# Optimization experiments

Measured on AMD Instinct MI355X. Metric: run time of the kernel, lower is better.

## Reference

```python
import jax, jax.numpy as jnp
import numpy as np

LEAK_RATE = 0.1
SPIKE_THRESHOLD = 0.5
MAX_DIM = 2560
R = 2048   # reservoir dim
D = 1024   # input dim
B = 4096   # batch


def setup_inputs() -> dict:
    key = jax.random.key(0)
    k1, k2, k3, k4, k5 = jax.random.split(key, 5)
    inputs = jax.random.normal(k1, (B, D), dtype=jnp.float32)
    prev_state = jax.random.normal(k2, (B, MAX_DIM), dtype=jnp.float32)
    W_in = jax.random.normal(k3, (R, D), dtype=jnp.float32) * (1.0 / np.sqrt(D))
    W_res = jax.random.normal(k4, (R, R), dtype=jnp.float32) * (1.0 / np.sqrt(R))
    W_gate = jax.random.normal(k5, (3 * R, D), dtype=jnp.float32) * (1.0 / np.sqrt(D))
    return {"inputs": inputs, "prev_state": prev_state,
            "W_in": W_in, "W_res": W_res, "W_gate": W_gate}


def reference(inputs, prev_state, W_in, W_res, W_gate):
    # Slice state to active reservoir width (W_res.shape[0] == R)
    prev = prev_state[:, :R]                                  # [B, R]
    input_part = jnp.matmul(inputs, W_in.T)                   # [B, R]
    reservoir_part = jnp.matmul(prev, W_res.T)                # [B, R]
    gate = jax.nn.sigmoid(jnp.matmul(inputs, W_gate.T))       # [B, 3R]
    i_gate, f_gate, o_gate = jnp.split(gate, 3, axis=-1)      # each [B, R]
    state = (1.0 - LEAK_RATE) * (f_gate * prev) \
        + LEAK_RATE * jnp.tanh(i_gate * (input_part + reservoir_part))
    state = o_gate * state
    # Spike threshold + soft reset
    state = jnp.where(state > SPIKE_THRESHOLD, state - SPIKE_THRESHOLD, state)
    # Pad up to max dynamic reservoir dim
    padded = jnp.pad(state, ((0, 0), (0, MAX_DIM - R)))       # [B, MAX_DIM]
    return padded
```

## Files before the change

kernel.cpp:

```cpp
#include <hip/hip_runtime.h>

#define B_  4096
#define D_  1024
#define R_  2048
#define MAXD 2560

typedef _Float16 half8 __attribute__((ext_vector_type(8)));
typedef _Float16 half4 __attribute__((ext_vector_type(4)));
typedef float    f32x4 __attribute__((ext_vector_type(4)));

constexpr int BM = 128;
constexpr int BN = 64;
constexpr int BK = 32;
constexpr int NCHUNK = (D_ + R_) / BK;
constexpr int NCH1   = D_ / BK;

__device__ __forceinline__ float sigmoidf_(float x) { return 1.0f / (1.0f + expf(-x)); }

__device__ __forceinline__ void wg_barrier() {
    __builtin_amdgcn_sched_barrier(0);
    asm volatile("s_waitcnt lgkmcnt(0)" ::: "memory");
    __builtin_amdgcn_s_barrier();
    __builtin_amdgcn_sched_barrier(0);
}

__global__ __launch_bounds__(256, 2)
void reservoir_fused(const float* __restrict__ X,
                     const float* __restrict__ P,
                     const float* __restrict__ Win,
                     const float* __restrict__ Wres,
                     const float* __restrict__ Wg,
                     float* __restrict__ out)
{
    __shared__ _Float16 sA[2][8][512];
    __shared__ _Float16 sW[2][4][4][512];

    const int tid  = threadIdx.x;
    const int lane = tid & 63;
    const int wv   = tid >> 6;
    const int m0   = blockIdx.y * BM;
    const int n0   = blockIdx.x * BN;

    f32x4 acc[4][2][4];
    #pragma unroll
    for (int s = 0; s < 4; ++s)
        #pragma unroll
        for (int mt = 0; mt < 2; ++mt)
            #pragma unroll
            for (int nt = 0; nt < 4; ++nt) acc[s][mt][nt] = (f32x4){0.f, 0.f, 0.f, 0.f};

    const int crow = tid >> 3;
    const int c4   = (tid & 7) * 4;
    const int q    = c4 >> 3;
    const int fbase = q * 128 + (c4 & 4);

    const int raddr = ((((lane & 15) ^ (lane >> 4)) << 3) + ((lane >> 4) << 7));

    f32x4 pa[4];
    f32x4 pw[8];

    auto issue_loads = [&](int t) {
        if (t < NCH1) {
            const int kc = t * BK + c4;
            const float* a = X + (size_t)m0 * D_ + kc;
            #pragma unroll
            for (int i = 0; i < 4; ++i)
                pa[i] = *(const f32x4*)(a + (size_t)(crow + 32 * i) * D_);
            const float* w = Win + (size_t)n0 * D_ + kc;
            #pragma unroll
            for (int i = 0; i < 2; ++i)
                pw[i] = *(const f32x4*)(w + (size_t)(crow + 32 * i) * D_);
            const float* g = Wg + (size_t)n0 * D_ + kc;
            #pragma unroll
            for (int gg = 0; gg < 3; ++gg)
                #pragma unroll
                for (int i = 0; i < 2; ++i)
                    pw[2 + gg * 2 + i] = *(const f32x4*)(g + (size_t)(gg * R_ + crow + 32 * i) * D_);
        } else {
            const int kc = t * BK - D_ + c4;
            const float* a = P + (size_t)m0 * MAXD + kc;
            #pragma unroll
            for (int i = 0; i < 4; ++i)
                pa[i] = *(const f32x4*)(a + (size_t)(crow + 32 * i) * MAXD);
            const float* w = Wres + (size_t)n0 * R_ + kc;
            #pragma unroll
            for (int i = 0; i < 2; ++i)
                pw[i] = *(const f32x4*)(w + (size_t)(crow + 32 * i) * R_);
        }
    };

    auto stage_A = [&]() {
        #pragma unroll
        for (int i = 0; i < 4; ++i) {
            const int r = crow + 32 * i;
            const int idx = (((r & 15) ^ q) << 3) + fbase;
            half4 h, l;
            #pragma unroll
            for (int j = 0; j < 4; ++j) {
                float v = pa[i][j];
                h[j] = (_Float16)v;
                l[j] = (_Float16)(v - (float)h[j]);
            }
            *(half4*)(&sA[0][r >> 4][idx]) = h;
            *(half4*)(&sA[1][r >> 4][idx]) = l;
        }
    };
    auto stage_W = [&](int nw) {
        #pragma unroll
        for (int i = 0; i < 8; ++i) if (i < nw) {
            const int s   = (i < 2) ? 0 : 1 + ((i - 2) >> 1);
            const int sub = (i < 2) ? i : ((i - 2) & 1);
            const int r   = crow + 32 * sub;
            const int idx = (((r & 15) ^ q) << 3) + fbase;
            half4 h, l;
            #pragma unroll
            for (int j = 0; j < 4; ++j) {
                float v = pw[i][j];
                h[j] = (_Float16)v;
                l[j] = (_Float16)(v - (float)h[j]);
            }
            *(half4*)(&sW[0][s][r >> 4][idx]) = h;
            *(half4*)(&sW[1][s][r >> 4][idx]) = l;
        }
    };

#define MFMA_BLOCK(NSETS)                                                                         \
    {                                                                                             \
        half8 ah0 = *(const half8*)(&sA[0][wv * 2 + 0][raddr]);                                   \
        half8 al0 = *(const half8*)(&sA[1][wv * 2 + 0][raddr]);                                   \
        half8 ah1 = *(const half8*)(&sA[0][wv * 2 + 1][raddr]);                                   \
        half8 al1 = *(const half8*)(&sA[1][wv * 2 + 1][raddr]);                                   \
        __builtin_amdgcn_s_setprio(1);                                                            \
        _Pragma("unroll")                                                                         \
        for (int s = 0; s < NSETS; ++s) {                                                         \
            _Pragma("unroll")                                                                     \
            for (int nt = 0; nt < 4; ++nt) {                                                      \
                half8 bh = *(const half8*)(&sW[0][s][nt][raddr]);                                 \
                half8 bl = *(const half8*)(&sW[1][s][nt][raddr]);                                 \
                acc[s][0][nt] = __builtin_amdgcn_mfma_f32_16x16x32_f16(ah0, bh, acc[s][0][nt], 0, 0, 0); \
                acc[s][0][nt] = __builtin_amdgcn_mfma_f32_16x16x32_f16(al0, bh, acc[s][0][nt], 0, 0, 0); \
                acc[s][0][nt] = __builtin_amdgcn_mfma_f32_16x16x32_f16(ah0, bl, acc[s][0][nt], 0, 0, 0); \
                acc[s][1][nt] = __builtin_amdgcn_mfma_f32_16x16x32_f16(ah1, bh, acc[s][1][nt], 0, 0, 0); \
                acc[s][1][nt] = __builtin_amdgcn_mfma_f32_16x16x32_f16(al1, bh, acc[s][1][nt], 0, 0, 0); \
                acc[s][1][nt] = __builtin_amdgcn_mfma_f32_16x16x32_f16(ah1, bl, acc[s][1][nt], 0, 0, 0); \
            }                                                                                     \
        }                                                                                         \
        __builtin_amdgcn_s_setprio(0);                                                            \
    }

    issue_loads(0);

    #pragma unroll 1
    for (int t = 0; t < NCH1; ++t) {
        stage_A();
        stage_W(8);
        issue_loads(t + 1);
        wg_barrier();
        MFMA_BLOCK(4)
        wg_barrier();
    }
    #pragma unroll 1
    for (int t = NCH1; t < NCHUNK; ++t) {
        stage_A();
        stage_W(2);
        if (t + 1 < NCHUNK) issue_loads(t + 1);
        wg_barrier();
        MFMA_BLOCK(1)
        wg_barrier();
    }
#undef MFMA_BLOCK

    const int fr = lane & 15;
    const int qd = lane >> 4;
    #pragma unroll
    for (int mt = 0; mt < 2; ++mt)
        #pragma unroll
        for (int nt = 0; nt < 4; ++nt)
            #pragma unroll
            for (int r = 0; r < 4; ++r) {
                int row = m0 + wv * 32 + mt * 16 + qd * 4 + r;
                int col = n0 + nt * 16 + fr;
                float pre = acc[0][mt][nt][r];
                float ig  = sigmoidf_(acc[1][mt][nt][r]);
                float fg  = sigmoidf_(acc[2][mt][nt][r]);
                float og  = sigmoidf_(acc[3][mt][nt][r]);
                float pv  = P[(size_t)row * MAXD + col];
                float st  = 0.9f * (fg * pv) + 0.1f * tanhf(ig * pre);
                st *= og;
                if (st > 0.5f) st -= 0.5f;
                out[(size_t)row * MAXD + col] = st;
            }
}

__global__ void pad_zero(float* __restrict__ out) {
    int idx = blockIdx.x * 256 + threadIdx.x;
    int row = idx >> 7;
    int c   = (idx & 127) * 4;
    *(f32x4*)(&out[(size_t)row * MAXD + R_ + c]) = (f32x4){0.f, 0.f, 0.f, 0.f};
}

extern "C" void kernel_launch(void* const* d_in, const int* in_sizes, int n_in,
                              void* d_out, int out_size, void* d_ws, size_t ws_size,
                              hipStream_t stream) {
    const float* X    = (const float*)d_in[0];
    const float* P    = (const float*)d_in[1];
    const float* Win  = (const float*)d_in[2];
    const float* Wres = (const float*)d_in[3];
    const float* Wg   = (const float*)d_in[4];
    float* out        = (float*)d_out;

    pad_zero<<<2048, 256, 0, stream>>>(out);
    dim3 grid(R_ / BN, B_ / BM);
    reservoir_fused<<<grid, 256, 0, stream>>>(X, P, Win, Wres, Wg, out);
}
```

Measured before the change: 436.8 us.

## Pre-split fp32 operands into packed fp16 hi/lo planes in a workspace pass

Adds a pre-pass kernel that converts X, the active slice of prev_state, W_in, W_res and W_gate into interleaved fp16 hi/lo pairs stored in the workspace. The fused GEMM then loads the packed pairs and writes them straight to shared memory, so the per-tile fp32-to-fp16 split no longer repeats across every block that reads the same operand. The cost is an extra kernel launch and a full read plus write of all operands, about 80 MB of traffic. The old path is kept as a fallback when the workspace is missing or too small.

```diff
diff --git a/kernel.cpp b/kernel.cpp
--- a/kernel.cpp
+++ b/kernel.cpp
@@ -8,6 +8,7 @@
 typedef _Float16 half8 __attribute__((ext_vector_type(8)));
 typedef _Float16 half4 __attribute__((ext_vector_type(4)));
 typedef float    f32x4 __attribute__((ext_vector_type(4)));
+typedef float    f32x2 __attribute__((ext_vector_type(2)));
 
 constexpr int BM = 128;
 constexpr int BN = 64;
@@ -15,6 +16,14 @@
 constexpr int NCHUNK = (D_ + R_) / BK;
 constexpr int NCH1   = D_ / BK;
 
+constexpr size_t XP_OFF   = 0;
+constexpr size_t PP_OFF   = XP_OFF   + (size_t)B_ * D_ / 4;
+constexpr size_t WINP_OFF = PP_OFF   + (size_t)B_ * R_ / 4;
+constexpr size_t WRESP_OFF= WINP_OFF + (size_t)R_ * D_ / 4;
+constexpr size_t WGP_OFF  = WRESP_OFF+ (size_t)R_ * R_ / 4;
+constexpr size_t WS_UNITS = WGP_OFF  + (size_t)3 * R_ * D_ / 4;
+constexpr size_t WS_BYTES = WS_UNITS * 16;
+
 __device__ __forceinline__ float sigmoidf_(float x) { return 1.0f / (1.0f + expf(-x)); }
 
 __device__ __forceinline__ void wg_barrier() {
@@ -24,12 +33,47 @@
     __builtin_amdgcn_sched_barrier(0);
 }
 
+__global__ __launch_bounds__(256)
+void pack_planes(const float* __restrict__ X, const float* __restrict__ P,
+                 const float* __restrict__ Win, const float* __restrict__ Wres,
+                 const float* __restrict__ Wg, f32x4* __restrict__ ws)
+{
+    size_t gid = (size_t)blockIdx.x * 256 + threadIdx.x;
+    if (gid >= WS_UNITS) return;
+    const float* src;
+    if (gid < PP_OFF) {
+        src = X + gid * 4;
+    } else if (gid < WINP_OFF) {
+        size_t s = gid - PP_OFF;
+        src = P + (s >> 9) * MAXD + (s & 511) * 4;
+    } else if (gid < WRESP_OFF) {
+        src = Win + (gid - WINP_OFF) * 4;
+    } else if (gid < WGP_OFF) {
+        src = Wres + (gid - WRESP_OFF) * 4;
+    } else {
+        src = Wg + (gid - WGP_OFF) * 4;
+    }
+    f32x4 v = *(const f32x4*)src;
+    half4 h, l;
+    #pragma unroll
+    for (int j = 0; j < 4; ++j) {
+        h[j] = (_Float16)v[j];
+        l[j] = (_Float16)(v[j] - (float)h[j]);
+    }
+    f32x4 o;
+    ((half4*)&o)[0] = h;
+    ((half4*)&o)[1] = l;
+    ws[gid] = o;
+}
+
+template<bool PACKED>
 __global__ __launch_bounds__(256, 2)
 void reservoir_fused(const float* __restrict__ X,
                      const float* __restrict__ P,
                      const float* __restrict__ Win,
                      const float* __restrict__ Wres,
                      const float* __restrict__ Wg,
+                     const f32x4* __restrict__ ws,
                      float* __restrict__ out)
 {
     __shared__ _Float16 sA[2][8][512];
@@ -62,30 +106,56 @@
     auto issue_loads = [&](int t) {
         if (t < NCH1) {
             const int kc = t * BK + c4;
-            const float* a = X + (size_t)m0 * D_ + kc;
-            #pragma unroll
-            for (int i = 0; i < 4; ++i)
-                pa[i] = *(const f32x4*)(a + (size_t)(crow + 32 * i) * D_);
-            const float* w = Win + (size_t)n0 * D_ + kc;
-            #pragma unroll
-            for (int i = 0; i < 2; ++i)
-                pw[i] = *(const f32x4*)(w + (size_t)(crow + 32 * i) * D_);
-            const float* g = Wg + (size_t)n0 * D_ + kc;
-            #pragma unroll
-            for (int gg = 0; gg < 3; ++gg)
+            if constexpr (PACKED) {
+                const int kq = kc >> 2;
+                const f32x4* a = ws + XP_OFF + (size_t)(m0 + crow) * (D_ / 4) + kq;
+                #pragma unroll
+                for (int i = 0; i < 4; ++i) pa[i] = a[(size_t)(32 * i) * (D_ / 4)];
+                const f32x4* w = ws + WINP_OFF + (size_t)(n0 + crow) * (D_ / 4) + kq;
+                #pragma unroll
+                for (int i = 0; i < 2; ++i) pw[i] = w[(size_t)(32 * i) * (D_ / 4)];
+                const f32x4* g = ws + WGP_OFF + (size_t)(n0 + crow) * (D_ / 4) + kq;
+                #pragma unroll
+                for (int gg = 0; gg < 3; ++gg)
+                    #pragma unroll
+                    for (int i = 0; i < 2; ++i)
+                        pw[2 + gg * 2 + i] = g[(size_t)(gg * R_ + 32 * i) * (D_ / 4)];
+            } else {
+                const float* a = X + (size_t)m0 * D_ + kc;
+                #pragma unroll
+                for (int i = 0; i < 4; ++i)
+                    pa[i] = *(const f32x4*)(a + (size_t)(crow + 32 * i) * D_);
+                const float* w = Win + (size_t)n0 * D_ + kc;
                 #pragma unroll
                 for (int i = 0; i < 2; ++i)
-                    pw[2 + gg * 2 + i] = *(const f32x4*)(g + (size_t)(gg * R_ + crow + 32 * i) * D_);
+                    pw[i] = *(const f32x4*)(w + (size_t)(crow + 32 * i) * D_);
+                const float* g = Wg + (size_t)n0 * D_ + kc;
+                #pragma unroll
+                for (int gg = 0; gg < 3; ++gg)
+                    #pragma unroll
+                    for (int i = 0; i < 2; ++i)
+                        pw[2 + gg * 2 + i] = *(const f32x4*)(g + (size_t)(gg * R_ + crow + 32 * i) * D_);
+            }
         } else {
             const int kc = t * BK - D_ + c4;
-            const float* a = P + (size_t)m0 * MAXD + kc;
-            #pragma unroll
-            for (int i = 0; i < 4; ++i)
-                pa[i] = *(const f32x4*)(a + (size_t)(crow + 32 * i) * MAXD);
-            const float* w = Wres + (size_t)n0 * R_ + kc;
-            #pragma unroll
-            for (int i = 0; i < 2; ++i)
-                pw[i] = *(const f32x4*)(w + (size_t)(crow + 32 * i) * R_);
+            if constexpr (PACKED) {
+                const int kq = kc >> 2;
+                const f32x4* a = ws + PP_OFF + (size_t)(m0 + crow) * (R_ / 4) + kq;
+                #pragma unroll
+                for (int i = 0; i < 4; ++i) pa[i] = a[(size_t)(32 * i) * (R_ / 4)];
+                const f32x4* w = ws + WRESP_OFF + (size_t)(n0 + crow) * (R_ / 4) + kq;
+                #pragma unroll
+                for (int i = 0; i < 2; ++i) pw[i] = w[(size_t)(32 * i) * (R_ / 4)];
+            } else {
+                const float* a = P + (size_t)m0 * MAXD + kc;
+                #pragma unroll
+                for (int i = 0; i < 4; ++i)
+                    pa[i] = *(const f32x4*)(a + (size_t)(crow + 32 * i) * MAXD);
+                const float* w = Wres + (size_t)n0 * R_ + kc;
+                #pragma unroll
+                for (int i = 0; i < 2; ++i)
+                    pw[i] = *(const f32x4*)(w + (size_t)(crow + 32 * i) * R_);
+            }
         }
     };
 
@@ -94,15 +164,21 @@
         for (int i = 0; i < 4; ++i) {
             const int r = crow + 32 * i;
             const int idx = (((r & 15) ^ q) << 3) + fbase;
-            half4 h, l;
-            #pragma unroll
-            for (int j = 0; j < 4; ++j) {
-                float v = pa[i][j];
-                h[j] = (_Float16)v;
-                l[j] = (_Float16)(v - (float)h[j]);
-            }
-            *(half4*)(&sA[0][r >> 4][idx]) = h;
-            *(half4*)(&sA[1][r >> 4][idx]) = l;
+            if constexpr (PACKED) {
+                f32x4 v = pa[i];
+                *(f32x2*)(&sA[0][r >> 4][idx]) = (f32x2){v.x, v.y};
+                *(f32x2*)(&sA[1][r >> 4][idx]) = (f32x2){v.z, v.w};
+            } else {
+                half4 h, l;
+                #pragma unroll
+                for (int j = 0; j < 4; ++j) {
+                    float v = pa[i][j];
+                    h[j] = (_Float16)v;
+                    l[j] = (_Float16)(v - (float)h[j]);
+                }
+                *(half4*)(&sA[0][r >> 4][idx]) = h;
+                *(half4*)(&sA[1][r >> 4][idx]) = l;
+            }
         }
     };
     auto stage_W = [&](int nw) {
@@ -112,15 +188,21 @@
             const int sub = (i < 2) ? i : ((i - 2) & 1);
             const int r   = crow + 32 * sub;
             const int idx = (((r & 15) ^ q) << 3) + fbase;
-            half4 h, l;
-            #pragma unroll
-            for (int j = 0; j < 4; ++j) {
-                float v = pw[i][j];
-                h[j] = (_Float16)v;
-                l[j] = (_Float16)(v - (float)h[j]);
-            }
-            *(half4*)(&sW[0][s][r >> 4][idx]) = h;
-            *(half4*)(&sW[1][s][r >> 4][idx]) = l;
+            if constexpr (PACKED) {
+                f32x4 v = pw[i];
+                *(f32x2*)(&sW[0][s][r >> 4][idx]) = (f32x2){v.x, v.y};
+                *(f32x2*)(&sW[1][s][r >> 4][idx]) = (f32x2){v.z, v.w};
+            } else {
+                half4 h, l;
+                #pragma unroll
+                for (int j = 0; j < 4; ++j) {
+                    float v = pw[i][j];
+                    h[j] = (_Float16)v;
+                    l[j] = (_Float16)(v - (float)h[j]);
+                }
+                *(half4*)(&sW[0][s][r >> 4][idx]) = h;
+                *(half4*)(&sW[1][s][r >> 4][idx]) = l;
+            }
         }
     };
 
@@ -211,5 +293,12 @@
 
     pad_zero<<<2048, 256, 0, stream>>>(out);
     dim3 grid(R_ / BN, B_ / BM);
-    reservoir_fused<<<grid, 256, 0, stream>>>(X, P, Win, Wres, Wg, out);
-}
+
+    if (d_ws != nullptr && ws_size >= WS_BYTES) {
+        f32x4* ws = (f32x4*)d_ws;
+        pack_planes<<<(int)(WS_UNITS / 256), 256, 0, stream>>>(X, P, Win, Wres, Wg, ws);
+        reservoir_fused<true><<<grid, 256, 0, stream>>>(X, P, Win, Wres, Wg, ws, out);
+    } else {
+        reservoir_fused<false><<<grid, 256, 0, stream>>>(X, P, Win, Wres, Wg, nullptr, out);
+    }
+}
```

After: 454.4 us. 4.0% more time.

## Pre-pack fp16 hi/lo operands into workspace and DMA weights directly into LDS

Applied to the files above, without the earlier changes.

A new prep kernel converts X, P and all weights into split fp16 hi/lo tiles already laid out in MFMA fragment order, and zeroes the output padding in the same launch. The main kernel then loads A fragments straight into registers and streams weight tiles into double-buffered LDS with global_load_lds. This removes the per-block fp32-to-fp16 conversion and the register-staged LDS stores from the main loop, and overlaps the next chunk's loads with the current MFMA work. The cost is an extra pass over all inputs plus workspace writes of roughly twice the fp32 volume in fp16 pairs. The old path is kept as a fallback for when no workspace is available.

```diff
diff --git a/kernel.cpp b/kernel.cpp
--- a/kernel.cpp
+++ b/kernel.cpp
@@ -1,4 +1,5 @@
 #include <hip/hip_runtime.h>
+#include <stdint.h>
 
 #define B_  4096
 #define D_  1024
@@ -12,34 +13,78 @@
 constexpr int BM = 128;
 constexpr int BN = 64;
 constexpr int BK = 32;
-constexpr int NCHUNK = (D_ + R_) / BK;
-constexpr int NCH1   = D_ / BK;
+constexpr int NCH1 = D_ / BK;
+constexpr int NCH2 = R_ / BK;
+
+constexpr size_t XF_OFF  = 0;
+constexpr size_t PF_OFF  = XF_OFF  + (size_t)256 * 32 * 2 * 512;
+constexpr size_t WIF_OFF = PF_OFF  + (size_t)256 * 64 * 2 * 512;
+constexpr size_t WRF_OFF = WIF_OFF + (size_t)128 * 32 * 2 * 512;
+constexpr size_t WGF_OFF = WRF_OFF + (size_t)128 * 64 * 2 * 512;
+constexpr size_t WS_HALVES = WGF_OFF + (size_t)384 * 32 * 2 * 512;
+constexpr size_t WS_BYTES  = WS_HALVES * 2;
+constexpr int NPACK_WTASKS = 49152;
+constexpr int NPAD_WTASKS  = 8192;
 
 __device__ __forceinline__ float sigmoidf_(float x) { return 1.0f / (1.0f + expf(-x)); }
 
-__device__ __forceinline__ void wg_barrier() {
-    __builtin_amdgcn_sched_barrier(0);
-    asm volatile("s_waitcnt lgkmcnt(0)" ::: "memory");
-    __builtin_amdgcn_s_barrier();
-    __builtin_amdgcn_sched_barrier(0);
+__device__ __forceinline__ void gload_lds16(const _Float16* g, _Float16* l) {
+    typedef const uint32_t __attribute__((address_space(1)))* gp_t;
+    typedef uint32_t __attribute__((address_space(3)))* lp_t;
+    __builtin_amdgcn_global_load_lds((gp_t)(const void*)g, (lp_t)(void*)l, 16, 0, 0);
+}
+
+__global__ __launch_bounds__(256)
+void prep(const float* __restrict__ X, const float* __restrict__ P,
+          const float* __restrict__ Win, const float* __restrict__ Wres,
+          const float* __restrict__ Wg, _Float16* __restrict__ ws,
+          float* __restrict__ out)
+{
+    const int l = threadIdx.x & 63;
+    const int wtask = blockIdx.x * 4 + (threadIdx.x >> 6);
+    if (wtask < NPACK_WTASKS) {
+        const float* src; int ld, rg, kb;
+        int cp = wtask;
+        if (cp < 8192)       {              src = X;    ld = D_;   rg = cp >> 5; kb = cp & 31; }
+        else if (cp < 24576) { cp -= 8192;  src = P;    ld = MAXD; rg = cp >> 6; kb = cp & 63; }
+        else if (cp < 28672) { cp -= 24576; src = Win;  ld = D_;   rg = cp >> 5; kb = cp & 31; }
+        else if (cp < 36864) { cp -= 28672; src = Wres; ld = R_;   rg = cp >> 6; kb = cp & 63; }
+        else                 { cp -= 36864; src = Wg;   ld = D_;   rg = cp >> 5; kb = cp & 31; }
+        const float* s = src + (size_t)(rg * 16 + (l & 15)) * ld + kb * 32 + (l >> 4) * 8;
+        f32x4 v0 = *(const f32x4*)s;
+        f32x4 v1 = *(const f32x4*)(s + 4);
+        half8 h, lo;
+        #pragma unroll
+        for (int j = 0; j < 4; ++j) {
+            h[j]     = (_Float16)v0[j];  lo[j]     = (_Float16)(v0[j] - (float)h[j]);
+            h[4 + j] = (_Float16)v1[j];  lo[4 + j] = (_Float16)(v1[j] - (float)h[4 + j]);
+        }
+        _Float16* dst = ws + (size_t)wtask * 1024;
+        *(half8*)(dst + l * 8) = h;
+        *(half8*)(dst + 512 + l * 8) = lo;
+    } else {
+        int p2 = wtask - NPACK_WTASKS;
+        size_t idx = (size_t)p2 * 256 + l * 4;
+        size_t row = idx >> 9, col = idx & 511;
+        *(f32x4*)(out + row * MAXD + R_ + col) = (f32x4){0.f, 0.f, 0.f, 0.f};
+    }
 }
 
 __global__ __launch_bounds__(256, 2)
-void reservoir_fused(const float* __restrict__ X,
-                     const float* __restrict__ P,
-                     const float* __restrict__ Win,
-                     const float* __restrict__ Wres,
-                     const float* __restrict__ Wg,
-                     float* __restrict__ out)
+void reservoir_packed(const _Float16* __restrict__ ws,
+                      const float* __restrict__ P,
+                      float* __restrict__ out)
 {
-    __shared__ _Float16 sA[2][8][512];
-    __shared__ _Float16 sW[2][4][4][512];
+    __shared__ _Float16 smem[32768];
 
     const int tid  = threadIdx.x;
     const int lane = tid & 63;
     const int wv   = tid >> 6;
     const int m0   = blockIdx.y * BM;
     const int n0   = blockIdx.x * BN;
+    const int lb   = lane * 8;
+    const int rgA  = (m0 >> 4) + wv * 2;
+    const int ng0  = n0 >> 4;
 
     f32x4 acc[4][2][4];
     #pragma unroll
@@ -49,27 +94,168 @@
             #pragma unroll
             for (int nt = 0; nt < 4; ++nt) acc[s][mt][nt] = (f32x4){0.f, 0.f, 0.f, 0.f};
 
+    auto dmaW1 = [&](int t, int buf) {
+        #pragma unroll
+        for (int i = 0; i < 8; ++i) {
+            const int c = wv * 8 + i, pl = c >> 4, r = c & 15, s = r >> 2, g = r & 3;
+            const size_t gh = (s == 0)
+                ? WIF_OFF + ((size_t)((ng0 + g) * 32 + t) * 2 + pl) * 512
+                : WGF_OFF + ((size_t)(((s - 1) * 128 + ng0 + g) * 32 + t) * 2 + pl) * 512;
+            gload_lds16(ws + gh + lb, &smem[buf * 16384 + pl * 8192 + r * 512]);
+        }
+    };
+    auto dmaW2 = [&](int t, int buf) {
+        #pragma unroll
+        for (int i = 0; i < 2; ++i) {
+            const int c = wv * 2 + i, pl = c >> 2, g = c & 3;
+            const size_t gh = WRF_OFF + ((size_t)((ng0 + g) * 64 + t) * 2 + pl) * 512;
+            gload_lds16(ws + gh + lb, &smem[buf * 16384 + pl * 8192 + g * 512]);
+        }
+    };
+
+#define LDA(ROFF, KBS, T, H0, L0, H1, L1)                                                         \
+    {                                                                                             \
+        const _Float16* b0_ = ws + (ROFF) + ((size_t)((rgA + 0) * (KBS) + (T)) * 2) * 512 + lb;   \
+        const _Float16* b1_ = ws + (ROFF) + ((size_t)((rgA + 1) * (KBS) + (T)) * 2) * 512 + lb;   \
+        H0 = *(const half8*)b0_;  L0 = *(const half8*)(b0_ + 512);                                \
+        H1 = *(const half8*)b1_;  L1 = *(const half8*)(b1_ + 512);                                \
+    }
+
+#define MBLK(BB, NSETS, AH0, AL0, AH1, AL1)                                                       \
+    {                                                                                             \
+        __builtin_amdgcn_s_setprio(1);                                                            \
+        _Pragma("unroll")                                                                         \
+        for (int s = 0; s < (NSETS); ++s) {                                                       \
+            _Pragma("unroll")                                                                     \
+            for (int nt = 0; nt < 4; ++nt) {                                                      \
+                half8 bh = *(const half8*)&smem[(BB) + (s * 4 + nt) * 512 + lb];                  \
+                half8 bl = *(const half8*)&smem[(BB) + 8192 + (s * 4 + nt) * 512 + lb];           \
+                acc[s][0][nt] = __builtin_amdgcn_mfma_f32_16x16x32_f16(AH0, bh, acc[s][0][nt], 0, 0, 0); \
+                acc[s][0][nt] = __builtin_amdgcn_mfma_f32_16x16x32_f16(AL0, bh, acc[s][0][nt], 0, 0, 0); \
+                acc[s][0][nt] = __builtin_amdgcn_mfma_f32_16x16x32_f16(AH0, bl, acc[s][0][nt], 0, 0, 0); \
+                acc[s][1][nt] = __builtin_amdgcn_mfma_f32_16x16x32_f16(AH1, bh, acc[s][1][nt], 0, 0, 0); \
+                acc[s][1][nt] = __builtin_amdgcn_mfma_f32_16x16x32_f16(AL1, bh, acc[s][1][nt], 0, 0, 0); \
+                acc[s][1][nt] = __builtin_amdgcn_mfma_f32_16x16x32_f16(AH1, bl, acc[s][1][nt], 0, 0, 0); \
+            }                                                                                     \
+        }                                                                                         \
+        __builtin_amdgcn_s_setprio(0);                                                            \
+    }
+
+#define BARR()                                                                                    \
+    {                                                                                             \
+        __builtin_amdgcn_sched_barrier(0);                                                        \
+        asm volatile("s_waitcnt vmcnt(4) lgkmcnt(0)" ::: "memory");                               \
+        __builtin_amdgcn_s_barrier();                                                             \
+        __builtin_amdgcn_sched_barrier(0);                                                        \
+    }
+#define FENCE() __builtin_amdgcn_sched_barrier(0)
+
+    half8 ah0A, al0A, ah1A, al1A, ah0B, al0B, ah1B, al1B;
+
+    dmaW1(0, 0);
+    FENCE();
+    LDA(XF_OFF, 32, 0, ah0A, al0A, ah1A, al1A);
+    BARR();
+
+    #pragma unroll 1
+    for (int t = 0; t < NCH1 - 2; t += 2) {
+        dmaW1(t + 1, 1); FENCE(); LDA(XF_OFF, 32, t + 1, ah0B, al0B, ah1B, al1B);
+        MBLK(0, 4, ah0A, al0A, ah1A, al1A)
+        BARR();
+        dmaW1(t + 2, 0); FENCE(); LDA(XF_OFF, 32, t + 2, ah0A, al0A, ah1A, al1A);
+        MBLK(16384, 4, ah0B, al0B, ah1B, al1B)
+        BARR();
+    }
+    dmaW1(31, 1); FENCE(); LDA(XF_OFF, 32, 31, ah0B, al0B, ah1B, al1B);
+    MBLK(0, 4, ah0A, al0A, ah1A, al1A)
+    BARR();
+    dmaW2(0, 0); FENCE(); LDA(PF_OFF, 64, 0, ah0A, al0A, ah1A, al1A);
+    MBLK(16384, 4, ah0B, al0B, ah1B, al1B)
+    BARR();
+
+    #pragma unroll 1
+    for (int t = 0; t < NCH2 - 2; t += 2) {
+        dmaW2(t + 1, 1); FENCE(); LDA(PF_OFF, 64, t + 1, ah0B, al0B, ah1B, al1B);
+        MBLK(0, 1, ah0A, al0A, ah1A, al1A)
+        BARR();
+        dmaW2(t + 2, 0); FENCE(); LDA(PF_OFF, 64, t + 2, ah0A, al0A, ah1A, al1A);
+        MBLK(16384, 1, ah0B, al0B, ah1B, al1B)
+        BARR();
+    }
+    dmaW2(63, 1); FENCE(); LDA(PF_OFF, 64, 63, ah0B, al0B, ah1B, al1B);
+    MBLK(0, 1, ah0A, al0A, ah1A, al1A)
+    BARR();
+    MBLK(16384, 1, ah0B, al0B, ah1B, al1B)
+
+#undef MBLK
+#undef LDA
+#undef BARR
+#undef FENCE
+
+    const int fr = lane & 15;
+    const int qd = lane >> 4;
+    #pragma unroll
+    for (int mt = 0; mt < 2; ++mt)
+        #pragma unroll
+        for (int nt = 0; nt < 4; ++nt)
+            #pragma unroll
+            for (int r = 0; r < 4; ++r) {
+                int row = m0 + wv * 32 + mt * 16 + qd * 4 + r;
+                int col = n0 + nt * 16 + fr;
+                float pre = acc[0][mt][nt][r];
+                float ig  = sigmoidf_(acc[1][mt][nt][r]);
+                float fg  = sigmoidf_(acc[2][mt][nt][r]);
+                float og  = sigmoidf_(acc[3][mt][nt][r]);
+                float pv  = P[(size_t)row * MAXD + col];
+                float st  = 0.9f * (fg * pv) + 0.1f * tanhf(ig * pre);
+                st *= og;
+                if (st > 0.5f) st -= 0.5f;
+                out[(size_t)row * MAXD + col] = st;
+            }
+}
+
+__device__ __forceinline__ void wg_barrier_ref() {
+    __builtin_amdgcn_sched_barrier(0);
+    asm volatile("s_waitcnt lgkmcnt(0)" ::: "memory");
+    __builtin_amdgcn_s_barrier();
+    __builtin_amdgcn_sched_barrier(0);
+}
+
+__global__ __launch_bounds__(256, 2)
+void reservoir_ref(const float* __restrict__ X, const float* __restrict__ P,
+                   const float* __restrict__ Win, const float* __restrict__ Wres,
+                   const float* __restrict__ Wg, float* __restrict__ out)
+{
+    __shared__ _Float16 sA[2][8][512];
+    __shared__ _Float16 sW[2][4][4][512];
+    const int tid  = threadIdx.x;
+    const int lane = tid & 63;
+    const int wv   = tid >> 6;
+    const int m0   = blockIdx.y * BM;
+    const int n0   = blockIdx.x * BN;
+    f32x4 acc[4][2][4];
+    #pragma unroll
+    for (int s = 0; s < 4; ++s)
+        #pragma unroll
+        for (int mt = 0; mt < 2; ++mt)
+            #pragma unroll
+            for (int nt = 0; nt < 4; ++nt) acc[s][mt][nt] = (f32x4){0.f, 0.f, 0.f, 0.f};
     const int crow = tid >> 3;
     const int c4   = (tid & 7) * 4;
     const int q    = c4 >> 3;
     const int fbase = q * 128 + (c4 & 4);
-
     const int raddr = ((((lane & 15) ^ (lane >> 4)) << 3) + ((lane >> 4) << 7));
-
     f32x4 pa[4];
     f32x4 pw[8];
-
     auto issue_loads = [&](int t) {
         if (t < NCH1) {
             const int kc = t * BK + c4;
             const float* a = X + (size_t)m0 * D_ + kc;
             #pragma unroll
-            for (int i = 0; i < 4; ++i)
-                pa[i] = *(const f32x4*)(a + (size_t)(crow + 32 * i) * D_);
+            for (int i = 0; i < 4; ++i) pa[i] = *(const f32x4*)(a + (size_t)(crow + 32 * i) * D_);
             const float* w = Win + (size_t)n0 * D_ + kc;
             #pragma unroll
-            for (int i = 0; i < 2; ++i)
-                pw[i] = *(const f32x4*)(w + (size_t)(crow + 32 * i) * D_);
+            for (int i = 0; i < 2; ++i) pw[i] = *(const f32x4*)(w + (size_t)(crow + 32 * i) * D_);
             const float* g = Wg + (size_t)n0 * D_ + kc;
             #pragma unroll
             for (int gg = 0; gg < 3; ++gg)
@@ -80,15 +266,12 @@
             const int kc = t * BK - D_ + c4;
             const float* a = P + (size_t)m0 * MAXD + kc;
             #pragma unroll
-            for (int i = 0; i < 4; ++i)
-                pa[i] = *(const f32x4*)(a + (size_t)(crow + 32 * i) * MAXD);
+            for (int i = 0; i < 4; ++i) pa[i] = *(const f32x4*)(a + (size_t)(crow + 32 * i) * MAXD);
             const float* w = Wres + (size_t)n0 * R_ + kc;
             #pragma unroll
-            for (int i = 0; i < 2; ++i)
-                pw[i] = *(const f32x4*)(w + (size_t)(crow + 32 * i) * R_);
-        }
-    };
-
+            for (int i = 0; i < 2; ++i) pw[i] = *(const f32x4*)(w + (size_t)(crow + 32 * i) * R_);
+        }
+    };
     auto stage_A = [&]() {
         #pragma unroll
         for (int i = 0; i < 4; ++i) {
@@ -123,14 +306,12 @@
             *(half4*)(&sW[1][s][r >> 4][idx]) = l;
         }
     };
-
-#define MFMA_BLOCK(NSETS)                                                                         \
+#define RMFMA(NSETS)                                                                              \
     {                                                                                             \
         half8 ah0 = *(const half8*)(&sA[0][wv * 2 + 0][raddr]);                                   \
         half8 al0 = *(const half8*)(&sA[1][wv * 2 + 0][raddr]);                                   \
         half8 ah1 = *(const half8*)(&sA[0][wv * 2 + 1][raddr]);                                   \
         half8 al1 = *(const half8*)(&sA[1][wv * 2 + 1][raddr]);                                   \
-        __builtin_amdgcn_s_setprio(1);                                                            \
         _Pragma("unroll")                                                                         \
         for (int s = 0; s < NSETS; ++s) {                                                         \
             _Pragma("unroll")                                                                     \
@@ -145,31 +326,25 @@
                 acc[s][1][nt] = __builtin_amdgcn_mfma_f32_16x16x32_f16(ah1, bl, acc[s][1][nt], 0, 0, 0); \
             }                                                                                     \
         }                                                                                         \
-        __builtin_amdgcn_s_setprio(0);                                                            \
-    }
-
+    }
     issue_loads(0);
-
     #pragma unroll 1
     for (int t = 0; t < NCH1; ++t) {
-        stage_A();
-        stage_W(8);
+        stage_A(); stage_W(8);
         issue_loads(t + 1);
-        wg_barrier();
-        MFMA_BLOCK(4)
-        wg_barrier();
+        wg_barrier_ref();
+        RMFMA(4)
+        wg_barrier_ref();
     }
     #pragma unroll 1
-    for (int t = NCH1; t < NCHUNK; ++t) {
-        stage_A();
-        stage_W(2);
-        if (t + 1 < NCHUNK) issue_loads(t + 1);
-        wg_barrier();
-        MFMA_BLOCK(1)
-        wg_barrier();
-    }
-#undef MFMA_BLOCK
-
+    for (int t = NCH1; t < NCH1 + NCH2; ++t) {
+        stage_A(); stage_W(2);
+        if (t + 1 < NCH1 + NCH2) issue_loads(t + 1);
+        wg_barrier_ref();
+        RMFMA(1)
+        wg_barrier_ref();
+    }
+#undef RMFMA
     const int fr = lane & 15;
     const int qd = lane >> 4;
     #pragma unroll
@@ -209,7 +384,14 @@
     const float* Wg   = (const float*)d_in[4];
     float* out        = (float*)d_out;
 
-    pad_zero<<<2048, 256, 0, stream>>>(out);
     dim3 grid(R_ / BN, B_ / BM);
-    reservoir_fused<<<grid, 256, 0, stream>>>(X, P, Win, Wres, Wg, out);
-}
+
+    if (d_ws != nullptr && ws_size >= WS_BYTES) {
+        _Float16* ws = (_Float16*)d_ws;
+        prep<<<(NPACK_WTASKS + NPAD_WTASKS) / 4, 256, 0, stream>>>(X, P, Win, Wres, Wg, ws, out);
+        reservoir_packed<<<grid, 256, 0, stream>>>((const _Float16*)ws, P, out);
+    } else {
+        pad_zero<<<2048, 256, 0, stream>>>(out);
+        reservoir_ref<<<grid, 256, 0, stream>>>(X, P, Win, Wres, Wg, out);
+    }
+}
```

Measured after the change: 421.9 us. 1.04x faster.
